# Kernel tuning notes

Measured on AMD Instinct MI355X. Metric: run time of the kernel, lower is better.

Reference implementation:

```python
import jax, jax.numpy as jnp
import numpy as np

_EPS = 1e-4  # pytorch3d se3_exp_map clamps the SQUARED rotation angle at this eps


def _hat(w):
    # w: [..., 3] -> skew-symmetric [..., 3, 3]
    wx, wy, wz = w[..., 0], w[..., 1], w[..., 2]
    z = jnp.zeros_like(wx)
    return jnp.stack([
        jnp.stack([z, -wz, wy], axis=-1),
        jnp.stack([wz, z, -wx], axis=-1),
        jnp.stack([-wy, wx, z], axis=-1),
    ], axis=-2)


def _se3_exp(dofs):
    # dofs: [..., 6] = (log_translation, log_rotation), pytorch3d convention.
    # Returns R [..., 3, 3] and t [..., 3] such that p' = R @ p + t,
    # matching pytorch3d's row-convention matrix M ([:3,:3]=R^T, [3,:3]=t)
    # applied as p' = p @ M[:3,:3] + M[3,:3].
    t_log = dofs[..., :3]
    w = dofs[..., 3:]
    nrms = jnp.sum(w * w, axis=-1)
    theta = jnp.sqrt(jnp.clip(nrms, _EPS))  # [...]
    H = _hat(w)
    H2 = H @ H
    st, ct = jnp.sin(theta), jnp.cos(theta)
    f1 = (st / theta)[..., None, None]
    f2 = ((1.0 - ct) / (theta * theta))[..., None, None]
    f3 = ((theta - st) / (theta * theta * theta))[..., None, None]
    I = jnp.eye(3, dtype=dofs.dtype)
    R = I + f1 * H + f2 * H2            # Rodrigues
    V = I + f2 * H + f3 * H2            # left-Jacobian of SO(3)
    t = jnp.einsum('...ij,...j->...i', V, t_log)
    return R, t


def setup_inputs() -> dict:
    key = jax.random.key(0)
    k1, k2 = jax.random.split(key)
    B, T, N = 64, 28, 4096
    X_v = jax.random.normal(k1, (B, T, N, 3), dtype=jnp.float32)
    dofs = jax.random.normal(k2, (B, T, 6), dtype=jnp.float32)
    return {"X_v": X_v, "dofs": dofs}


def reference(X_v, dofs):
    # Fused, fully-batched version of the per-tooth python loop:
    # one SE3 exp over all (B,T) transforms + one batched point transform.
    R, t = _se3_exp(dofs)                                  # [B,T,3,3], [B,T,3]
    out = jnp.einsum('btij,btnj->btni', R, X_v) + t[:, :, None, :]
    return out
```

## Files before the change

kernel.cpp:

```cpp
#include <hip/hip_runtime.h>


#define LDS_FENCE() asm volatile("s_waitcnt lgkmcnt(0)" ::: "memory")

__global__ __launch_bounds__(256) void se3_apply_kernel(
    const float* __restrict__ X,
    const float* __restrict__ dofs,
    float* __restrict__ out,
    int n3)
{
    __shared__ float lds[3072];

    const int bt   = blockIdx.x;
    const int lane = threadIdx.x & 63;
    const int w    = threadIdx.x >> 6;

    const float* d = dofs + bt * 6;
    const float tx = d[0], ty = d[1], tz = d[2];
    const float wx = d[3], wy = d[4], wz = d[5];

    const float nrm2  = wx * wx + wy * wy + wz * wz;
    const float th2   = fmaxf(nrm2, 1e-4f);
    const float theta = sqrtf(th2);
    const float st = sinf(theta);
    const float ct = cosf(theta);
    const float f1 = st / theta;
    const float f2 = (1.0f - ct) / th2;
    const float f3 = (theta - st) / (th2 * theta);

    const float xx = wx * wx, yy = wy * wy, zz = wz * wz;
    const float xy = wx * wy, xz = wx * wz, yz = wy * wz;

    const float R00 = 1.0f - f2 * (yy + zz);
    const float R01 = f2 * xy - f1 * wz;
    const float R02 = f2 * xz + f1 * wy;
    const float R10 = f2 * xy + f1 * wz;
    const float R11 = 1.0f - f2 * (xx + zz);
    const float R12 = f2 * yz - f1 * wx;
    const float R20 = f2 * xz - f1 * wy;
    const float R21 = f2 * yz + f1 * wx;
    const float R22 = 1.0f - f2 * (xx + yy);

    const float V00 = 1.0f - f3 * (yy + zz);
    const float V01 = f3 * xy - f2 * wz;
    const float V02 = f3 * xz + f2 * wy;
    const float V10 = f3 * xy + f2 * wz;
    const float V11 = 1.0f - f3 * (xx + zz);
    const float V12 = f3 * yz - f2 * wx;
    const float V20 = f3 * xz - f2 * wy;
    const float V21 = f3 * yz + f2 * wx;
    const float V22 = 1.0f - f3 * (xx + yy);

    const float Tx = V00 * tx + V01 * ty + V02 * tz;
    const float Ty = V10 * tx + V11 * ty + V12 * tz;
    const float Tz = V20 * tx + V21 * ty + V22 * tz;

    const long long btBase = (long long)bt * (long long)n3;
    float* const wlds   = lds + w * 768;
    float4* const wlds4 = (float4*)wlds;

    const int nChunks = n3 / 768;

    float4 v0, v1, v2;
    {
        const float4* __restrict__ g4 = (const float4*)(X + btBase + (long long)w * 768);
        v0 = g4[lane];
        v1 = g4[lane + 64];
        v2 = g4[lane + 128];
    }

    for (int c = w; c < nChunks; c += 4) {
        const long long base = btBase + (long long)c * 768;
        float4* __restrict__ o4 = (float4*)(out + base);

        wlds4[lane]       = v0;
        wlds4[lane + 64]  = v1;
        wlds4[lane + 128] = v2;
        LDS_FENCE();

        const int cn = c + 4;
        if (cn < nChunks) {
            const float4* __restrict__ gn = (const float4*)(X + btBase + (long long)cn * 768);
            v0 = gn[lane];
            v1 = gn[lane + 64];
            v2 = gn[lane + 128];
        }

#pragma unroll
        for (int j = 0; j < 4; ++j) {
            const int p = 3 * (lane + 64 * j);
            const float px = wlds[p + 0];
            const float py = wlds[p + 1];
            const float pz = wlds[p + 2];
            wlds[p + 0] = fmaf(R00, px, fmaf(R01, py, fmaf(R02, pz, Tx)));
            wlds[p + 1] = fmaf(R10, px, fmaf(R11, py, fmaf(R12, pz, Ty)));
            wlds[p + 2] = fmaf(R20, px, fmaf(R21, py, fmaf(R22, pz, Tz)));
        }
        LDS_FENCE();

        o4[lane]       = wlds4[lane];
        o4[lane + 64]  = wlds4[lane + 64];
        o4[lane + 128] = wlds4[lane + 128];
        LDS_FENCE();
    }

    const int tailF = n3 - nChunks * 768;
    if (tailF > 0 && w == 0) {
        const int tailPts = tailF / 3;
        const long long tbase = btBase + (long long)nChunks * 768;
        for (int p = lane; p < tailPts; p += 64) {
            const float px = X[tbase + 3 * p + 0];
            const float py = X[tbase + 3 * p + 1];
            const float pz = X[tbase + 3 * p + 2];
            out[tbase + 3 * p + 0] = fmaf(R00, px, fmaf(R01, py, fmaf(R02, pz, Tx)));
            out[tbase + 3 * p + 1] = fmaf(R10, px, fmaf(R11, py, fmaf(R12, pz, Ty)));
            out[tbase + 3 * p + 2] = fmaf(R20, px, fmaf(R21, py, fmaf(R22, pz, Tz)));
        }
    }
}

extern "C" void kernel_launch(void* const* d_in, const int* in_sizes, int n_in,
                              void* d_out, int out_size, void* d_ws, size_t ws_size,
                              hipStream_t stream) {
    const float* X    = (const float*)d_in[0];
    const float* dofs = (const float*)d_in[1];
    float* out        = (float*)d_out;

    const int BT = in_sizes[1] / 6;
    const int n3 = in_sizes[0] / BT;

    dim3 grid((unsigned)BT);
    se3_apply_kernel<<<grid, 256, 0, stream>>>(X, dofs, out, n3);
}
```

Measured before the change: 158.9 us.

## Use direct global-to-LDS DMA double buffering with nontemporal stores

Global loads of X go straight into LDS through global_load_lds with two LDS buffers per wave, so the next chunk streams in while the current one is transformed. Explicit vmcnt waits stand in for the register round trip. Output stores are marked nontemporal, and the block shrinks to 128 threads (2 waves), each handling alternate chunks. With only 1792 blocks of 2 waves, the GPU holds fewer waves in flight to hide memory latency, and the exact vmcnt accounting plus cross-lane LDS visibility are fragile.

```diff
diff --git a/kernel.cpp b/kernel.cpp
--- a/kernel.cpp
+++ b/kernel.cpp
@@ -1,9 +1,24 @@
 #include <hip/hip_runtime.h>
 
 
+#define VMCNT3()    asm volatile("s_waitcnt vmcnt(3)" ::: "memory")
+#define VMCNT0()    asm volatile("s_waitcnt vmcnt(0)" ::: "memory")
 #define LDS_FENCE() asm volatile("s_waitcnt lgkmcnt(0)" ::: "memory")
 
-__global__ __launch_bounds__(256) void se3_apply_kernel(
+typedef float vfloat4 __attribute__((ext_vector_type(4)));
+
+typedef __attribute__((address_space(3))) void       as3_void;
+typedef const __attribute__((address_space(1))) void as1_void;
+
+__device__ __forceinline__ void dma_chunk(const float* gp_lane,
+                                          float* ldsbase)
+{
+    __builtin_amdgcn_global_load_lds((as1_void*)(gp_lane),       (as3_void*)(ldsbase),       16, 0, 0);
+    __builtin_amdgcn_global_load_lds((as1_void*)(gp_lane + 256), (as3_void*)(ldsbase + 256), 16, 0, 0);
+    __builtin_amdgcn_global_load_lds((as1_void*)(gp_lane + 512), (as3_void*)(ldsbase + 512), 16, 0, 0);
+}
+
+__global__ __launch_bounds__(128) void se3_apply_kernel(
     const float* __restrict__ X,
     const float* __restrict__ dofs,
     float* __restrict__ out,
@@ -56,57 +71,51 @@
     const float Tz = V20 * tx + V21 * ty + V22 * tz;
 
     const long long btBase = (long long)bt * (long long)n3;
-    float* const wlds   = lds + w * 768;
-    float4* const wlds4 = (float4*)wlds;
+    const float* const gX = X + btBase;
+
+    float* const buf0 = lds + w * 1536;
+    float* const buf1 = buf0 + 768;
 
     const int nChunks = n3 / 768;
 
-    float4 v0, v1, v2;
-    {
-        const float4* __restrict__ g4 = (const float4*)(X + btBase + (long long)w * 768);
-        v0 = g4[lane];
-        v1 = g4[lane + 64];
-        v2 = g4[lane + 128];
-    }
+    if (w < nChunks)
+        dma_chunk(gX + (long long)w * 768 + lane * 4, buf0);
 
-    for (int c = w; c < nChunks; c += 4) {
-        const long long base = btBase + (long long)c * 768;
-        float4* __restrict__ o4 = (float4*)(out + base);
+    for (int c = w, it = 0; c < nChunks; c += 2, ++it) {
+        float* const cur = (it & 1) ? buf1 : buf0;
+        float* const nxt = (it & 1) ? buf0 : buf1;
 
-        wlds4[lane]       = v0;
-        wlds4[lane + 64]  = v1;
-        wlds4[lane + 128] = v2;
-        LDS_FENCE();
-
-        const int cn = c + 4;
+        const int cn = c + 2;
         if (cn < nChunks) {
-            const float4* __restrict__ gn = (const float4*)(X + btBase + (long long)cn * 768);
-            v0 = gn[lane];
-            v1 = gn[lane + 64];
-            v2 = gn[lane + 128];
+            dma_chunk(gX + (long long)cn * 768 + lane * 4, nxt);
+            VMCNT3();
+        } else {
+            VMCNT0();
         }
 
 #pragma unroll
         for (int j = 0; j < 4; ++j) {
             const int p = 3 * (lane + 64 * j);
-            const float px = wlds[p + 0];
-            const float py = wlds[p + 1];
-            const float pz = wlds[p + 2];
-            wlds[p + 0] = fmaf(R00, px, fmaf(R01, py, fmaf(R02, pz, Tx)));
-            wlds[p + 1] = fmaf(R10, px, fmaf(R11, py, fmaf(R12, pz, Ty)));
-            wlds[p + 2] = fmaf(R20, px, fmaf(R21, py, fmaf(R22, pz, Tz)));
+            const float px = cur[p + 0];
+            const float py = cur[p + 1];
+            const float pz = cur[p + 2];
+            cur[p + 0] = fmaf(R00, px, fmaf(R01, py, fmaf(R02, pz, Tx)));
+            cur[p + 1] = fmaf(R10, px, fmaf(R11, py, fmaf(R12, pz, Ty)));
+            cur[p + 2] = fmaf(R20, px, fmaf(R21, py, fmaf(R22, pz, Tz)));
         }
         LDS_FENCE();
 
-        o4[lane]       = wlds4[lane];
-        o4[lane + 64]  = wlds4[lane + 64];
-        o4[lane + 128] = wlds4[lane + 128];
+        vfloat4* const o4 = (vfloat4*)(out + btBase + (long long)c * 768);
+        const vfloat4* const c4 = (const vfloat4*)cur;
+        __builtin_nontemporal_store(c4[lane],       o4 + lane);
+        __builtin_nontemporal_store(c4[lane + 64],  o4 + lane + 64);
+        __builtin_nontemporal_store(c4[lane + 128], o4 + lane + 128);
         LDS_FENCE();
     }
 
-    const int tailF = n3 - nChunks * 768;
-    if (tailF > 0 && w == 0) {
-        const int tailPts = tailF / 3;
+    const int nTail = n3 - nChunks * 768;
+    if (nTail > 0 && w == 0) {
+        const int tailPts = nTail / 3;
         const long long tbase = btBase + (long long)nChunks * 768;
         for (int p = lane; p < tailPts; p += 64) {
             const float px = X[tbase + 3 * p + 0];
@@ -130,5 +139,5 @@
     const int n3 = in_sizes[0] / BT;
 
     dim3 grid((unsigned)BT);
-    se3_apply_kernel<<<grid, 256, 0, stream>>>(X, dofs, out, n3);
+    se3_apply_kernel<<<grid, 128, 0, stream>>>(X, dofs, out, n3);
 }
```

Measured after the change: 162.1 us. 1.02x slower.
